# Performance work log

Hardware: AMD Instinct MI355X
Metric: run time of the kernel (lower is better)

The kernel has to match this reference:

```python
import jax, jax.numpy as jnp
import numpy as np

NM = 4096; NP = 4096; EM = 65536; EP = 65536; H = 256; HEADS = 4; G = 32


def _lin(k, din, dout):
    k1, k2 = jax.random.split(k)
    return (jax.random.normal(k1, (din, dout), jnp.float32) * (1.0 / np.sqrt(din)),
            jax.random.normal(k2, (dout,), jnp.float32) * 0.01)


def setup_inputs() -> dict:
    key = jax.random.key(0)
    ks = jax.random.split(key, 32)
    inp = {}
    inp['x_mol'] = jax.random.normal(ks[0], (NM, 8), jnp.float32)
    inp['x_prot'] = jax.random.normal(ks[1], (NP, 4), jnp.float32)
    inp['ea_mol'] = jax.random.normal(ks[2], (EM, 2), jnp.float32)
    inp['ea_prot'] = jax.random.normal(ks[3], (EP, 2), jnp.float32)
    inp['ei_mol'] = jax.random.randint(ks[4], (2, EM), 0, NM)
    inp['ei_prot'] = jax.random.randint(ks[5], (2, EP), 0, NP)
    inp['batch_mol'] = jnp.sort(jax.random.randint(ks[6], (NM,), 0, G))
    inp['batch_prot'] = jnp.sort(jax.random.randint(ks[7], (NP,), 0, G))
    inp['node_lin_mol_w'], inp['node_lin_mol_b'] = _lin(ks[8], 8, H)
    inp['node_lin_prot_w'], inp['node_lin_prot_b'] = _lin(ks[9], 4, H)
    inp['edge_lin_mol_w'], inp['edge_lin_mol_b'] = _lin(ks[10], 2, H)
    inp['edge_lin_prot_w'], inp['edge_lin_prot_b'] = _lin(ks[11], 2, H)
    # two GINE conv layers per graph, each with a 2-layer MLP; stack layer dim first
    for pref, base in (('mol', 12), ('prot', 16)):
        w1 = []; b1 = []; w2 = []; b2 = []
        for l in range(2):
            w, b = _lin(ks[base + 2 * l], H, H); w1.append(w); b1.append(b)
            w, b = _lin(ks[base + 2 * l + 1], H, H); w2.append(w); b2.append(b)
        inp[pref + '_w1'] = jnp.stack(w1); inp[pref + '_b1'] = jnp.stack(b1)
        inp[pref + '_w2'] = jnp.stack(w2); inp[pref + '_b2'] = jnp.stack(b2)
    for pref, base in (('mp', 20), ('pm', 23)):
        inp[pref + '_wq'], inp[pref + '_bq'] = _lin(ks[base], H, H)
        inp[pref + '_wk'], inp[pref + '_bk'] = _lin(ks[base + 1], H, H)
        inp[pref + '_wv'], inp[pref + '_bv'] = _lin(ks[base + 2], H, H)
    inp['fc1_w'], inp['fc1_b'] = _lin(ks[26], 2 * H, H)
    inp['fc2_w'], inp['fc2_b'] = _lin(ks[27], H, 1)
    return inp


def _gine_stack(x, ei, e, w1, b1, w2, b2):
    # GINEConv (eps=0): x_i' = relu(nn(x_i + sum_j relu(x_j + e_ji))), 2 layers, shared edge emb
    src, dst = ei[0], ei[1]
    n = x.shape[0]
    for l in range(w1.shape[0]):
        msg = jax.nn.relu(x[src] + e)                      # [E, H]
        agg = jax.ops.segment_sum(msg, dst, num_segments=n)  # [N, H]
        h = x + agg
        h = jax.nn.relu(h @ w1[l] + b1[l]) @ w2[l] + b2[l]
        x = jax.nn.relu(h)
    return x


def _cross_attn(qn, kn, wq, bq, wk, bk, wv, bv):
    nq, d = qn.shape
    nk = kn.shape[0]
    hd = d // HEADS
    Q = (qn @ wq + bq).reshape(nq, HEADS, hd)
    K = (kn @ wk + bk).reshape(nk, HEADS, hd)
    V = (kn @ wv + bv).reshape(nk, HEADS, hd)
    scores = jnp.einsum('qhd,khd->hqk', Q, K) / np.float32(hd ** 0.5)
    w = jax.nn.softmax(scores, axis=-1)
    return jnp.einsum('hqk,khd->qhd', w, V).reshape(nq, d)


def _seg_mean(h, seg, n):
    s = jax.ops.segment_sum(h, seg, num_segments=n)
    c = jax.ops.segment_sum(jnp.ones((h.shape[0], 1), h.dtype), seg, num_segments=n)
    return s / jnp.maximum(c, 1.0)


def reference(x_mol, x_prot, ea_mol, ea_prot, ei_mol, ei_prot, batch_mol, batch_prot,
              node_lin_mol_w, node_lin_mol_b, node_lin_prot_w, node_lin_prot_b,
              edge_lin_mol_w, edge_lin_mol_b, edge_lin_prot_w, edge_lin_prot_b,
              mol_w1, mol_b1, mol_w2, mol_b2, prot_w1, prot_b1, prot_w2, prot_b2,
              mp_wq, mp_bq, mp_wk, mp_bk, mp_wv, mp_bv,
              pm_wq, pm_bq, pm_wk, pm_bk, pm_wv, pm_bv,
              fc1_w, fc1_b, fc2_w, fc2_b):
    hm = x_mol @ node_lin_mol_w + node_lin_mol_b
    hp = x_prot @ node_lin_prot_w + node_lin_prot_b
    em = ea_mol @ edge_lin_mol_w + edge_lin_mol_b
    ep = ea_prot @ edge_lin_prot_w + edge_lin_prot_b
    H_mol = _gine_stack(hm, ei_mol, em, mol_w1, mol_b1, mol_w2, mol_b2)
    H_prot = _gine_stack(hp, ei_prot, ep, prot_w1, prot_b1, prot_w2, prot_b2)
    H_mol_c = H_mol + _cross_attn(H_mol, H_prot, mp_wq, mp_bq, mp_wk, mp_bk, mp_wv, mp_bv)
    H_prot_c = H_prot + _cross_attn(H_prot, H_mol, pm_wq, pm_bq, pm_wk, pm_bk, pm_wv, pm_bv)
    z_mol = _seg_mean(H_mol_c, batch_mol, G)
    z_prot = _seg_mean(H_prot_c, batch_prot, G)
    z = jnp.concatenate([z_mol, z_prot], axis=1)
    x = jax.nn.relu(z @ fc1_w + fc1_b)
    out = jax.nn.sigmoid(x @ fc2_w + fc2_b)
    return out.squeeze(-1)
```

## Files before the change

kernel.cpp:

```cpp
#include <hip/hip_runtime.h>
#include <math.h>

#define HDIM 256
#define NMOL 4096
#define NPROT 4096
#define NEDGE 65536
#define NG 32

typedef _Float16 f16x8 __attribute__((ext_vector_type(8)));
typedef _Float16 f16x4 __attribute__((ext_vector_type(4)));
typedef __attribute__((ext_vector_type(4))) float f32x4;

__device__ __forceinline__ void splitf(float x, _Float16& h, _Float16& l) {
  h = (_Float16)x;
  l = (_Float16)(x - (float)h);
}

struct PtrPack { const float* p[14]; };

__global__ __launch_bounds__(256) void k_prep_wt(PtrPack pk, _Float16* __restrict__ dh,
                                                 _Float16* __restrict__ dl) {
  __shared__ float Ts[64][68];
  const int m = blockIdx.z;
  const int n0 = blockIdx.y * 64, k0 = blockIdx.x * 64;
  const float* W = pk.p[m];
  const int t = threadIdx.x;
#pragma unroll
  for (int rep = 0; rep < 16; ++rep) {
    int k = rep * 4 + (t >> 6);
    int n = t & 63;
    Ts[n][k] = W[(size_t)(k0 + k) * 256 + n0 + n];
  }
  __syncthreads();
#pragma unroll
  for (int rep = 0; rep < 2; ++rep) {
    int idx = t + rep * 256;
    int nr = idx >> 3, koff = (idx & 7) * 8;
    f16x8 vh, vl;
#pragma unroll
    for (int i = 0; i < 8; ++i) {
      _Float16 h, l;
      splitf(Ts[nr][koff + i], h, l);
      vh[i] = h; vl[i] = l;
    }
    size_t off = (size_t)m * 65536 + (size_t)(n0 + nr) * 256 + k0 + koff;
    *(f16x8*)&dh[off] = vh;
    *(f16x8*)&dl[off] = vl;
  }
}

struct EmbJob { const float* x; const float* w; const float* b; float* out; int K; };

__global__ __launch_bounds__(256) void k_node_embed2(EmbJob j0, EmbJob j1) {
  const EmbJob& j = blockIdx.y ? j1 : j0;
  const int i = blockIdx.x;
  const int c = threadIdx.x;
  float acc = j.b[c];
  for (int k = 0; k < j.K; ++k) acc += j.x[i * j.K + k] * j.w[k * HDIM + c];
  j.out[(size_t)i * HDIM + c] = acc;
}

__global__ __launch_bounds__(256) void k_csr_count2(const int* __restrict__ ei0,
                                                    const int* __restrict__ ei1,
                                                    int* __restrict__ cur0,
                                                    int* __restrict__ cur1, int E) {
  const int* ei = blockIdx.y ? ei1 : ei0;
  int* cur = blockIdx.y ? cur1 : cur0;
  const int e = blockIdx.x * 256 + threadIdx.x;
  if (e < E) atomicAdd(&cur[ei[E + e]], 1);
}

__global__ __launch_bounds__(256) void k_csr_scan2(int* __restrict__ c0, int* __restrict__ o0,
                                                   int* __restrict__ c1, int* __restrict__ o1,
                                                   int N) {
  int* cnt_cur = blockIdx.x ? c1 : c0;
  int* off = blockIdx.x ? o1 : o0;
  __shared__ int tsum[256], tpre[257];
  const int t = threadIdx.x;
  const int base = t * 16;
  int loc[16], s = 0;
#pragma unroll
  for (int i = 0; i < 16; ++i) { loc[i] = cnt_cur[base + i]; s += loc[i]; }
  tsum[t] = s;
  __syncthreads();
  if (t == 0) {
    int a = 0;
    for (int i = 0; i < 256; ++i) { tpre[i] = a; a += tsum[i]; }
    tpre[256] = a;
  }
  __syncthreads();
  int a = tpre[t];
#pragma unroll
  for (int i = 0; i < 16; ++i) {
    off[base + i] = a;
    cnt_cur[base + i] = a;
    a += loc[i];
  }
  if (t == 255) off[N] = tpre[256];
}

__global__ __launch_bounds__(256) void k_csr_scatter2(const int* __restrict__ ei0,
                                                      const int* __restrict__ ei1,
                                                      int* __restrict__ cur0,
                                                      int* __restrict__ cur1,
                                                      int* __restrict__ eid0,
                                                      int* __restrict__ eid1, int E) {
  const int* ei = blockIdx.y ? ei1 : ei0;
  int* cur = blockIdx.y ? cur1 : cur0;
  int* eid = blockIdx.y ? eid1 : eid0;
  const int e = blockIdx.x * 256 + threadIdx.x;
  if (e < E) {
    int pos = atomicAdd(&cur[ei[E + e]], 1);
    eid[pos] = e;
  }
}

struct AggJob {
  const float* x; const float* ea; const int* eis; const int* off;
  const int* eid; const float* we; const float* be; float* agg;
};

__global__ __launch_bounds__(256) void k_agg2(AggJob a0, AggJob a1) {
  const AggJob& a = blockIdx.y ? a1 : a0;
  const int n = blockIdx.x;
  const int c = threadIdx.x;
  const float w0 = a.we[c], w1 = a.we[HDIM + c], bb = a.be[c];
  const int j0 = a.off[n], j1 = a.off[n + 1];
  float sum = 0.f;
  for (int j = j0; j < j1; ++j) {
    int e = a.eid[j];
    int src = a.eis[e];
    float e0 = a.ea[2 * e], e1 = a.ea[2 * e + 1];
    float m = a.x[(size_t)src * HDIM + c] + e0 * w0 + e1 * w1 + bb;
    sum += fmaxf(m, 0.f);
  }
  a.agg[(size_t)n * HDIM + c] = sum;
}

struct GJob {
  const float* A1; const float* A2;
  const _Float16* Ah; const _Float16* Al;
  const _Float16* Bh; const _Float16* Bl;
  const float* bias; float* C;
  _Float16* Ch; _Float16* Cl;
  float oscale; int flags;
};
struct GJobs { GJob j[6]; };

__global__ __launch_bounds__(256) void k_gemm(GJobs js) {
  const GJob J = js.j[blockIdx.z];
  const int relu = J.flags & 1, hasa2 = J.flags & 2, presplit = J.flags & 4;
  const int outmode = J.flags >> 4;
  __shared__ _Float16 Ah[64][72], Al[64][72], Bh[64][72], Bl[64][72];
  const int t = threadIdx.x;
  const int bm = blockIdx.x * 64, bn = blockIdx.y * 64;
  const int lane = t & 63, w = t >> 6;
  const int l15 = lane & 15, l4 = lane >> 4;
  const int wm = (w >> 1) * 32, wn = (w & 1) * 32;
  f32x4 acc[2][2] = {};
  for (int k0 = 0; k0 < 256; k0 += 64) {
    __syncthreads();
    if (presplit) {
#pragma unroll
      for (int rep = 0; rep < 2; ++rep) {
        int idx = t + rep * 256;
        int r = idx >> 3, k8 = (idx & 7) * 8;
        size_t off = (size_t)(bm + r) * 256 + k0 + k8;
        *(f16x8*)&Ah[r][k8] = *(const f16x8*)&J.Ah[off];
        *(f16x8*)&Al[r][k8] = *(const f16x8*)&J.Al[off];
      }
    } else {
#pragma unroll
      for (int rep = 0; rep < 4; ++rep) {
        int idx = t + rep * 256;
        int r = idx >> 4, c4 = (idx & 15) * 4;
        float4 a = *(const float4*)&J.A1[(size_t)(bm + r) * 256 + k0 + c4];
        if (hasa2) {
          float4 a2 = *(const float4*)&J.A2[(size_t)(bm + r) * 256 + k0 + c4];
          a.x += a2.x; a.y += a2.y; a.z += a2.z; a.w += a2.w;
        }
        float av[4] = {a.x, a.y, a.z, a.w};
#pragma unroll
        for (int i = 0; i < 4; ++i) splitf(av[i], Ah[r][c4 + i], Al[r][c4 + i]);
      }
    }
#pragma unroll
    for (int rep = 0; rep < 2; ++rep) {
      int idx = t + rep * 256;
      int nr = idx >> 3, koff = (idx & 7) * 8;
      size_t off = (size_t)(bn + nr) * 256 + k0 + koff;
      *(f16x8*)&Bh[nr][koff] = *(const f16x8*)&J.Bh[off];
      *(f16x8*)&Bl[nr][koff] = *(const f16x8*)&J.Bl[off];
    }
    __syncthreads();
#pragma unroll
    for (int kh = 0; kh < 2; ++kh) {
      f16x8 a0h = *(f16x8*)&Ah[wm + l15][kh * 32 + l4 * 8];
      f16x8 a0l = *(f16x8*)&Al[wm + l15][kh * 32 + l4 * 8];
      f16x8 a1h = *(f16x8*)&Ah[wm + 16 + l15][kh * 32 + l4 * 8];
      f16x8 a1l = *(f16x8*)&Al[wm + 16 + l15][kh * 32 + l4 * 8];
      f16x8 b0h = *(f16x8*)&Bh[wn + l15][kh * 32 + l4 * 8];
      f16x8 b0l = *(f16x8*)&Bl[wn + l15][kh * 32 + l4 * 8];
      f16x8 b1h = *(f16x8*)&Bh[wn + 16 + l15][kh * 32 + l4 * 8];
      f16x8 b1l = *(f16x8*)&Bl[wn + 16 + l15][kh * 32 + l4 * 8];
      acc[0][0] = __builtin_amdgcn_mfma_f32_16x16x32_f16(a0h, b0h, acc[0][0], 0, 0, 0);
      acc[0][0] = __builtin_amdgcn_mfma_f32_16x16x32_f16(a0h, b0l, acc[0][0], 0, 0, 0);
      acc[0][0] = __builtin_amdgcn_mfma_f32_16x16x32_f16(a0l, b0h, acc[0][0], 0, 0, 0);
      acc[0][1] = __builtin_amdgcn_mfma_f32_16x16x32_f16(a0h, b1h, acc[0][1], 0, 0, 0);
      acc[0][1] = __builtin_amdgcn_mfma_f32_16x16x32_f16(a0h, b1l, acc[0][1], 0, 0, 0);
      acc[0][1] = __builtin_amdgcn_mfma_f32_16x16x32_f16(a0l, b1h, acc[0][1], 0, 0, 0);
      acc[1][0] = __builtin_amdgcn_mfma_f32_16x16x32_f16(a1h, b0h, acc[1][0], 0, 0, 0);
      acc[1][0] = __builtin_amdgcn_mfma_f32_16x16x32_f16(a1h, b0l, acc[1][0], 0, 0, 0);
      acc[1][0] = __builtin_amdgcn_mfma_f32_16x16x32_f16(a1l, b0h, acc[1][0], 0, 0, 0);
      acc[1][1] = __builtin_amdgcn_mfma_f32_16x16x32_f16(a1h, b1h, acc[1][1], 0, 0, 0);
      acc[1][1] = __builtin_amdgcn_mfma_f32_16x16x32_f16(a1h, b1l, acc[1][1], 0, 0, 0);
      acc[1][1] = __builtin_amdgcn_mfma_f32_16x16x32_f16(a1l, b1h, acc[1][1], 0, 0, 0);
    }
  }
#pragma unroll
  for (int mi = 0; mi < 2; ++mi)
#pragma unroll
    for (int ni = 0; ni < 2; ++ni) {
      int col = bn + wn + ni * 16 + l15;
      float bv = J.bias[col];
#pragma unroll
      for (int r = 0; r < 4; ++r) {
        int row = bm + wm + mi * 16 + l4 * 4 + r;
        float v = acc[mi][ni][r] + bv;
        if (relu) v = fmaxf(v, 0.f);
        if (outmode != 1) J.C[(size_t)row * 256 + col] = v;
        if (outmode != 0) {
          float vs = v * J.oscale;
          _Float16 hh, ll;
          splitf(vs, hh, ll);
          J.Ch[(size_t)row * 256 + col] = hh;
          J.Cl[(size_t)row * 256 + col] = ll;
        }
      }
    }
}

__global__ __launch_bounds__(256) void k_transpose2(
    const float* __restrict__ V0, const float* __restrict__ V1,
    _Float16* __restrict__ Th0, _Float16* __restrict__ Th1) {
  __shared__ float Ts[64][65];
  const int dir = blockIdx.z;
  const float* V = dir ? V1 : V0;
  _Float16* Th = dir ? Th1 : Th0;
  const int r0 = blockIdx.x * 64, c0 = blockIdx.y * 64;
  const int t = threadIdx.x;
#pragma unroll
  for (int rep = 0; rep < 16; ++rep) {
    int idx = rep * 256 + t;
    int r = idx >> 6, c = idx & 63;
    Ts[r][c] = V[(size_t)(r0 + r) * 256 + c0 + c];
  }
  __syncthreads();
#pragma unroll
  for (int rep = 0; rep < 2; ++rep) {
    int idx = rep * 256 + t;
    int c = idx >> 3, r8 = (idx & 7) * 8;
    f16x8 vh;
#pragma unroll
    for (int i = 0; i < 8; ++i) vh[i] = (_Float16)Ts[r8 + i][c];
    *(f16x8*)&Th[(size_t)(c0 + c) * 4096 + r0 + r8] = vh;
  }
}

struct AttnArgs {
  const _Float16* Qh[2]; const _Float16* Ql[2];
  const _Float16* Kh[2]; const _Float16* Kl[2];
  const _Float16* Vth[2];
  float* Opart; float* mpart; float* lpart;
};

__global__ __launch_bounds__(256) void k_attn4(AttnArgs A, int nk_half) {
  __shared__ _Float16 Ksh[64][72], Ksl[64][72];
  __shared__ _Float16 Vsh[64][72];
  __shared__ _Float16 Psh[4][16][72];
  const int t = threadIdx.x;
  const int dir = blockIdx.y >> 2, h = blockIdx.y & 3;
  const int q0 = blockIdx.x * 64;
  const int half = blockIdx.z;
  const int kbase = half * nk_half;
  const int lane = t & 63, w = t >> 6;
  const int l15 = lane & 15, l4 = lane >> 4;

  const _Float16* Qh_g = A.Qh[dir];
  const _Float16* Ql_g = A.Ql[dir];
  const _Float16* Kh_g = A.Kh[dir];
  const _Float16* Kl_g = A.Kl[dir];
  const _Float16* Vth_g = A.Vth[dir];

  f16x8 qh[2], ql[2];
  {
    size_t qoff = (size_t)(q0 + w * 16 + l15) * 256 + h * 64;
#pragma unroll
    for (int kh = 0; kh < 2; ++kh) {
      qh[kh] = *(const f16x8*)&Qh_g[qoff + kh * 32 + l4 * 8];
      ql[kh] = *(const f16x8*)&Ql_g[qoff + kh * 32 + l4 * 8];
    }
  }
  f32x4 o[4] = {};
  float mrun = -1e30f;
  float lrun = 0.f;

  for (int kt = 0; kt < nk_half; kt += 64) {
    const int k0 = kbase + kt;
    __syncthreads();
#pragma unroll
    for (int rep = 0; rep < 2; ++rep) {
      int idx = t + rep * 256;
      int r = idx >> 3, c8 = idx & 7;
      size_t koff = (size_t)(k0 + r) * 256 + h * 64 + c8 * 8;
      *(f16x8*)&Ksh[r][c8 * 8] = *(const f16x8*)&Kh_g[koff];
      *(f16x8*)&Ksl[r][c8 * 8] = *(const f16x8*)&Kl_g[koff];
      int sc = c8 ^ ((r >> 3) & 7);
      size_t voff = (size_t)(h * 64 + r) * 4096 + k0 + c8 * 8;
      *(f16x8*)&Vsh[r][sc * 8] = *(const f16x8*)&Vth_g[voff];
    }
    __syncthreads();

    f32x4 sf[4] = {};
#pragma unroll
    for (int kc = 0; kc < 4; ++kc) {
      f16x8 kf0h = *(f16x8*)&Ksh[kc * 16 + l15][l4 * 8];
      f16x8 kf0l = *(f16x8*)&Ksl[kc * 16 + l15][l4 * 8];
      f16x8 kf1h = *(f16x8*)&Ksh[kc * 16 + l15][32 + l4 * 8];
      f16x8 kf1l = *(f16x8*)&Ksl[kc * 16 + l15][32 + l4 * 8];
      sf[kc] = __builtin_amdgcn_mfma_f32_16x16x32_f16(kf0h, qh[0], sf[kc], 0, 0, 0);
      sf[kc] = __builtin_amdgcn_mfma_f32_16x16x32_f16(kf0h, ql[0], sf[kc], 0, 0, 0);
      sf[kc] = __builtin_amdgcn_mfma_f32_16x16x32_f16(kf0l, qh[0], sf[kc], 0, 0, 0);
      sf[kc] = __builtin_amdgcn_mfma_f32_16x16x32_f16(kf1h, qh[1], sf[kc], 0, 0, 0);
      sf[kc] = __builtin_amdgcn_mfma_f32_16x16x32_f16(kf1h, ql[1], sf[kc], 0, 0, 0);
      sf[kc] = __builtin_amdgcn_mfma_f32_16x16x32_f16(kf1l, qh[1], sf[kc], 0, 0, 0);
    }

    float mt = -1e30f;
#pragma unroll
    for (int kc = 0; kc < 4; ++kc) {
      float a = fmaxf(fmaxf(sf[kc][0], sf[kc][1]), fmaxf(sf[kc][2], sf[kc][3]));
      mt = fmaxf(mt, a);
    }
    mt = fmaxf(mt, __shfl_xor(mt, 16, 64));
    mt = fmaxf(mt, __shfl_xor(mt, 32, 64));
    float mn = fmaxf(mrun, mt);
    float alpha = __expf(mrun - mn);
    mrun = mn;
    float rs = 0.f;
    _Float16 pf[4][4];
#pragma unroll
    for (int kc = 0; kc < 4; ++kc)
#pragma unroll
      for (int r = 0; r < 4; ++r) {
        float pv = __expf(sf[kc][r] - mn);
        rs += pv;
        pf[kc][r] = (_Float16)pv;
      }
    rs += __shfl_xor(rs, 16, 64);
    rs += __shfl_xor(rs, 32, 64);
    lrun = lrun * alpha + rs;

#pragma unroll
    for (int r = 0; r < 4; ++r) {
      float ar = __shfl(alpha, 4 * l4 + r, 64);
      o[0][r] *= ar; o[1][r] *= ar; o[2][r] *= ar; o[3][r] *= ar;
    }

#pragma unroll
    for (int kc = 0; kc < 4; ++kc) {
      f16x4 pv = {pf[kc][0], pf[kc][1], pf[kc][2], pf[kc][3]};
      *(f16x4*)&Psh[w][l15][kc * 16 + 4 * l4] = pv;
    }

#pragma unroll
    for (int kh = 0; kh < 2; ++kh) {
      f16x8 pa = *(f16x8*)&Psh[w][l15][kh * 32 + l4 * 8];
#pragma unroll
      for (int oc = 0; oc < 4; ++oc) {
        int d = oc * 16 + l15;
        int chunk = (kh * 4 + l4) ^ ((d >> 3) & 7);
        f16x8 vb = *(f16x8*)&Vsh[d][chunk * 8];
        o[oc] = __builtin_amdgcn_mfma_f32_16x16x32_f16(pa, vb, o[oc], 0, 0, 0);
      }
    }
  }

  const int slot = dir * 2 + half;
#pragma unroll
  for (int oc = 0; oc < 4; ++oc) {
    int col = h * 64 + oc * 16 + l15;
#pragma unroll
    for (int r = 0; r < 4; ++r) {
      int row = q0 + w * 16 + 4 * l4 + r;
      A.Opart[((size_t)slot * 4096 + row) * 256 + col] = o[oc][r];
    }
  }
  if (lane < 16) {
    int row = q0 + w * 16 + l15;
    A.mpart[(size_t)(slot * 4 + h) * 4096 + row] = mrun;
    A.lpart[(size_t)(slot * 4 + h) * 4096 + row] = lrun;
  }
}

__global__ __launch_bounds__(256) void k_combine_pool(
    const float* __restrict__ Opart, const float* __restrict__ mpart,
    const float* __restrict__ lpart, const float* __restrict__ hm,
    const float* __restrict__ hp, const int* __restrict__ b_mol,
    const int* __restrict__ b_prot, float* __restrict__ z, float* __restrict__ cnt) {
  const int row = blockIdx.x;
  const int dir = blockIdx.y;
  const int c = threadIdx.x;
  const int h = c >> 6;
  const float* Hin = dir ? hp : hm;
  const int g = (dir ? b_prot : b_mol)[row];
  size_t mi0 = (size_t)((dir * 2 + 0) * 4 + h) * 4096 + row;
  size_t mi1 = (size_t)((dir * 2 + 1) * 4 + h) * 4096 + row;
  float m1 = mpart[mi0], m2 = mpart[mi1];
  float l1 = lpart[mi0], l2 = lpart[mi1];
  float M = fmaxf(m1, m2);
  float e1 = __expf(m1 - M), e2 = __expf(m2 - M);
  float L = l1 * e1 + l2 * e2;
  float O1 = Opart[((size_t)(dir * 2 + 0) * 4096 + row) * 256 + c];
  float O2 = Opart[((size_t)(dir * 2 + 1) * 4096 + row) * 256 + c];
  float v = (O1 * e1 + O2 * e2) / L + Hin[(size_t)row * 256 + c];
  atomicAdd(&z[(size_t)g * 512 + dir * 256 + c], v);
  if (c == 0) atomicAdd(&cnt[dir * 32 + g], 1.0f);
}

__global__ __launch_bounds__(256) void k_segdiv(float* __restrict__ z,
                                                const float* __restrict__ cnt) {
  const int idx = blockIdx.x * 256 + threadIdx.x;
  const int g = idx >> 9, c = idx & 511;
  const float cc = cnt[(c < 256) ? g : (32 + g)];
  z[idx] /= fmaxf(cc, 1.0f);
}

__global__ __launch_bounds__(256) void k_fc1(
    const float* __restrict__ z, const float* __restrict__ w,
    const float* __restrict__ b, float* __restrict__ out) {
  const int idx = blockIdx.x * 256 + threadIdx.x;
  const int r = idx >> 8, c = idx & 255;
  float acc = b[c];
  for (int k = 0; k < 512; ++k) acc += z[r * 512 + k] * w[k * HDIM + c];
  out[idx] = fmaxf(acc, 0.f);
}

__global__ __launch_bounds__(64) void k_fc2(
    const float* __restrict__ xin, const float* __restrict__ w,
    const float* __restrict__ b, float* __restrict__ out) {
  const int r = threadIdx.x;
  if (r < NG) {
    float acc = b[0];
    for (int k = 0; k < HDIM; ++k) acc += xin[r * HDIM + k] * w[k];
    out[r] = 1.0f / (1.0f + __expf(-acc));
  }
}

extern "C" void kernel_launch(void* const* d_in, const int* in_sizes, int n_in,
                              void* d_out, int out_size, void* d_ws, size_t ws_size,
                              hipStream_t stream) {
  const float* x_mol   = (const float*)d_in[0];
  const float* x_prot  = (const float*)d_in[1];
  const float* ea_mol  = (const float*)d_in[2];
  const float* ea_prot = (const float*)d_in[3];
  const int*   ei_mol  = (const int*)d_in[4];
  const int*   ei_prot = (const int*)d_in[5];
  const int*   b_mol   = (const int*)d_in[6];
  const int*   b_prot  = (const int*)d_in[7];
  const float* nlm_w = (const float*)d_in[8];
  const float* nlm_b = (const float*)d_in[9];
  const float* nlp_w = (const float*)d_in[10];
  const float* nlp_b = (const float*)d_in[11];
  const float* elm_w = (const float*)d_in[12];
  const float* elm_b = (const float*)d_in[13];
  const float* elp_w = (const float*)d_in[14];
  const float* elp_b = (const float*)d_in[15];
  const float* mol_w1 = (const float*)d_in[16];
  const float* mol_b1 = (const float*)d_in[17];
  const float* mol_w2 = (const float*)d_in[18];
  const float* mol_b2 = (const float*)d_in[19];
  const float* prot_w1 = (const float*)d_in[20];
  const float* prot_b1 = (const float*)d_in[21];
  const float* prot_w2 = (const float*)d_in[22];
  const float* prot_b2 = (const float*)d_in[23];
  const float* mp_wq = (const float*)d_in[24];
  const float* mp_bq = (const float*)d_in[25];
  const float* mp_wk = (const float*)d_in[26];
  const float* mp_bk = (const float*)d_in[27];
  const float* mp_wv = (const float*)d_in[28];
  const float* mp_bv = (const float*)d_in[29];
  const float* pm_wq = (const float*)d_in[30];
  const float* pm_bq = (const float*)d_in[31];
  const float* pm_wk = (const float*)d_in[32];
  const float* pm_bk = (const float*)d_in[33];
  const float* pm_wv = (const float*)d_in[34];
  const float* pm_bv = (const float*)d_in[35];
  const float* fc1_w = (const float*)d_in[36];
  const float* fc1_b = (const float*)d_in[37];
  const float* fc2_w = (const float*)d_in[38];
  const float* fc2_b = (const float*)d_in[39];
  float* out = (float*)d_out;

  char* W8 = (char*)d_ws;
  const size_t MB = 1u << 20;
  float* hm    = (float*)(W8 + 0 * MB);
  float* hp    = (float*)(W8 + 4 * MB);
  float* t1m   = (float*)(W8 + 8 * MB);
  float* aggm  = (float*)(W8 + 12 * MB);
  float* aggp  = (float*)(W8 + 16 * MB);
  _Float16* wtH = (_Float16*)(W8 + 20 * MB);
  _Float16* wtL = (_Float16*)(W8 + 22 * MB);
  _Float16* hmh = (_Float16*)(W8 + 24 * MB);
  _Float16* hml = (_Float16*)(W8 + 26 * MB);
  _Float16* hph = (_Float16*)(W8 + 28 * MB);
  _Float16* hpl = (_Float16*)(W8 + 30 * MB);
  _Float16* Qh0 = (_Float16*)(W8 + 32 * MB);
  _Float16* Ql0 = (_Float16*)(W8 + 34 * MB);
  _Float16* Kh0 = (_Float16*)(W8 + 36 * MB);
  _Float16* Kl0 = (_Float16*)(W8 + 38 * MB);
  _Float16* Qh1 = (_Float16*)(W8 + 40 * MB);
  _Float16* Ql1 = (_Float16*)(W8 + 42 * MB);
  _Float16* Kh1 = (_Float16*)(W8 + 44 * MB);
  _Float16* Kl1 = (_Float16*)(W8 + 46 * MB);
  float* Vb0   = (float*)(W8 + 48 * MB);
  float* Vb1   = (float*)(W8 + 52 * MB);
  _Float16* Vth0 = (_Float16*)(W8 + 56 * MB);
  _Float16* Vth1 = (_Float16*)(W8 + 60 * MB);
  float* Opart = (float*)(W8 + 64 * MB);
  float* mpart = (float*)(W8 + 80 * MB);
  float* lpart = mpart + 65536;
  float* zb    = lpart + 65536;
  float* cnt   = zb + 32 * 512;
  float* fch   = cnt + 64;
  float* t1p   = (float*)(W8 + 82 * MB);
  int* off_m = (int*)(W8 + 86 * MB);
  int* cur_m = off_m + 4224;
  int* eid_m = cur_m + 4224;
  int* off_p = (int*)(W8 + 87 * MB);
  int* cur_p = off_p + 4224;
  int* eid_p = cur_p + 4224;

  PtrPack pk;
  pk.p[0] = mol_w1;           pk.p[1] = mol_w1 + 65536;
  pk.p[2] = mol_w2;           pk.p[3] = mol_w2 + 65536;
  pk.p[4] = prot_w1;          pk.p[5] = prot_w1 + 65536;
  pk.p[6] = prot_w2;          pk.p[7] = prot_w2 + 65536;
  pk.p[8] = mp_wq;  pk.p[9] = mp_wk;  pk.p[10] = mp_wv;
  pk.p[11] = pm_wq; pk.p[12] = pm_wk; pk.p[13] = pm_wv;
  k_prep_wt<<<dim3(4, 4, 14), 256, 0, stream>>>(pk, wtH, wtL);

  hipMemsetAsync(cur_m, 0, 4096 * 4, stream);
  hipMemsetAsync(cur_p, 0, 4096 * 4, stream);
  k_csr_count2<<<dim3(NEDGE / 256, 2), 256, 0, stream>>>(ei_mol, ei_prot, cur_m, cur_p, NEDGE);
  k_csr_scan2<<<2, 256, 0, stream>>>(cur_m, off_m, cur_p, off_p, NMOL);
  k_csr_scatter2<<<dim3(NEDGE / 256, 2), 256, 0, stream>>>(ei_mol, ei_prot, cur_m, cur_p,
                                                           eid_m, eid_p, NEDGE);

  EmbJob em = {x_mol, nlm_w, nlm_b, hm, 8};
  EmbJob ep = {x_prot, nlp_w, nlp_b, hp, 4};
  k_node_embed2<<<dim3(NMOL, 2), 256, 0, stream>>>(em, ep);

#define WTH(i) (wtH + (size_t)(i) * 65536)
#define WTL(i) (wtL + (size_t)(i) * 65536)

  AggJob am = {hm, ea_mol, ei_mol, off_m, eid_m, elm_w, elm_b, aggm};
  AggJob ap = {hp, ea_prot, ei_prot, off_p, eid_p, elp_w, elp_b, aggp};

  for (int l = 0; l < 2; ++l) {
    k_agg2<<<dim3(NMOL, 2), 256, 0, stream>>>(am, ap);
    GJobs g1 = {};
    g1.j[0] = {hm, aggm, nullptr, nullptr, WTH(l), WTL(l), mol_b1 + l * 256,
               t1m, nullptr, nullptr, 1.0f, 3};
    g1.j[1] = {hp, aggp, nullptr, nullptr, WTH(4 + l), WTL(4 + l), prot_b1 + l * 256,
               t1p, nullptr, nullptr, 1.0f, 3};
    k_gemm<<<dim3(64, 4, 2), 256, 0, stream>>>(g1);
    GJobs g2 = {};
    int fl = (l == 1) ? (1 | (2 << 4)) : 1;
    g2.j[0] = {t1m, nullptr, nullptr, nullptr, WTH(2 + l), WTL(2 + l), mol_b2 + l * 256,
               hm, hmh, hml, 1.0f, fl};
    g2.j[1] = {t1p, nullptr, nullptr, nullptr, WTH(6 + l), WTL(6 + l), prot_b2 + l * 256,
               hp, hph, hpl, 1.0f, fl};
    k_gemm<<<dim3(64, 4, 2), 256, 0, stream>>>(g2);
  }

  {
    GJobs q = {};
    q.j[0] = {nullptr, nullptr, hmh, hml, WTH(8), WTL(8), mp_bq,
              nullptr, Qh0, Ql0, 0.125f, 4 | (1 << 4)};
    q.j[1] = {nullptr, nullptr, hph, hpl, WTH(9), WTL(9), mp_bk,
              nullptr, Kh0, Kl0, 1.0f, 4 | (1 << 4)};
    q.j[2] = {nullptr, nullptr, hph, hpl, WTH(10), WTL(10), mp_bv,
              Vb0, nullptr, nullptr, 1.0f, 4};
    q.j[3] = {nullptr, nullptr, hph, hpl, WTH(11), WTL(11), pm_bq,
              nullptr, Qh1, Ql1, 0.125f, 4 | (1 << 4)};
    q.j[4] = {nullptr, nullptr, hmh, hml, WTH(12), WTL(12), pm_bk,
              nullptr, Kh1, Kl1, 1.0f, 4 | (1 << 4)};
    q.j[5] = {nullptr, nullptr, hmh, hml, WTH(13), WTL(13), pm_bv,
              Vb1, nullptr, nullptr, 1.0f, 4};
    k_gemm<<<dim3(64, 4, 6), 256, 0, stream>>>(q);
  }

  k_transpose2<<<dim3(64, 4, 2), 256, 0, stream>>>(Vb0, Vb1, Vth0, Vth1);

  AttnArgs aa;
  aa.Qh[0] = Qh0; aa.Ql[0] = Ql0; aa.Kh[0] = Kh0; aa.Kl[0] = Kl0; aa.Vth[0] = Vth0;
  aa.Qh[1] = Qh1; aa.Ql[1] = Ql1; aa.Kh[1] = Kh1; aa.Kl[1] = Kl1; aa.Vth[1] = Vth1;
  aa.Opart = Opart; aa.mpart = mpart; aa.lpart = lpart;
  k_attn4<<<dim3(64, 8, 2), 256, 0, stream>>>(aa, 2048);

  hipMemsetAsync(zb, 0, (32 * 512 + 64) * 4, stream);
  k_combine_pool<<<dim3(4096, 2), 256, 0, stream>>>(Opart, mpart, lpart, hm, hp,
                                                    b_mol, b_prot, zb, cnt);
  k_segdiv<<<64, 256, 0, stream>>>(zb, cnt);
  k_fc1<<<32, 256, 0, stream>>>(zb, fc1_w, fc1_b, fch);
  k_fc2<<<1, 64, 0, stream>>>(fch, fc2_w, fc2_b, out);
#undef WTH
#undef WTL
}
```

Before: 546.0 us.

## Keep activations in split fp16 hi/lo form and fuse V transpose into GEMM

Node features, aggregation results and MLP intermediates are now stored as fp16 hi/lo pairs instead of fp32. The GEMM therefore always loads presplit operands and drops the fp32 split path. The self-term addition moves into the aggregation kernel. The V projection writes its transposed fp16 output directly through shared memory, which removes the separate transpose kernel and the fp32 V buffers. This cuts global traffic and one launch, at the cost of extra conversion arithmetic in the gather loop and a small precision change from hi/lo reconstruction.

```diff
diff --git a/kernel.cpp b/kernel.cpp
--- a/kernel.cpp
+++ b/kernel.cpp
@@ -49,7 +49,10 @@
   }
 }
 
-struct EmbJob { const float* x; const float* w; const float* b; float* out; int K; };
+struct EmbJob {
+  const float* x; const float* w; const float* b;
+  _Float16* oh; _Float16* ol; int K;
+};
 
 __global__ __launch_bounds__(256) void k_node_embed2(EmbJob j0, EmbJob j1) {
   const EmbJob& j = blockIdx.y ? j1 : j0;
@@ -57,7 +60,10 @@
   const int c = threadIdx.x;
   float acc = j.b[c];
   for (int k = 0; k < j.K; ++k) acc += j.x[i * j.K + k] * j.w[k * HDIM + c];
-  j.out[(size_t)i * HDIM + c] = acc;
+  _Float16 h, l;
+  splitf(acc, h, l);
+  j.oh[(size_t)i * HDIM + c] = h;
+  j.ol[(size_t)i * HDIM + c] = l;
 }
 
 __global__ __launch_bounds__(256) void k_csr_count2(const int* __restrict__ ei0,
@@ -116,8 +122,10 @@
 }
 
 struct AggJob {
-  const float* x; const float* ea; const int* eis; const int* off;
-  const int* eid; const float* we; const float* be; float* agg;
+  const _Float16* xh; const _Float16* xl; const float* ea;
+  const int* eis; const int* off; const int* eid;
+  const float* we; const float* be;
+  _Float16* sh; _Float16* sl;
 };
 
 __global__ __launch_bounds__(256) void k_agg2(AggJob a0, AggJob a1) {
@@ -131,25 +139,29 @@
     int e = a.eid[j];
     int src = a.eis[e];
     float e0 = a.ea[2 * e], e1 = a.ea[2 * e + 1];
-    float m = a.x[(size_t)src * HDIM + c] + e0 * w0 + e1 * w1 + bb;
+    float xv = (float)a.xh[(size_t)src * HDIM + c] + (float)a.xl[(size_t)src * HDIM + c];
+    float m = xv + e0 * w0 + e1 * w1 + bb;
     sum += fmaxf(m, 0.f);
   }
-  a.agg[(size_t)n * HDIM + c] = sum;
+  float self = (float)a.xh[(size_t)n * HDIM + c] + (float)a.xl[(size_t)n * HDIM + c];
+  _Float16 h, l;
+  splitf(self + sum, h, l);
+  a.sh[(size_t)n * HDIM + c] = h;
+  a.sl[(size_t)n * HDIM + c] = l;
 }
 
 struct GJob {
-  const float* A1; const float* A2;
   const _Float16* Ah; const _Float16* Al;
   const _Float16* Bh; const _Float16* Bl;
-  const float* bias; float* C;
-  _Float16* Ch; _Float16* Cl;
+  const float* bias;
+  _Float16* Ch; _Float16* Cl; _Float16* Vt;
   float oscale; int flags;
 };
 struct GJobs { GJob j[6]; };
 
 __global__ __launch_bounds__(256) void k_gemm(GJobs js) {
   const GJob J = js.j[blockIdx.z];
-  const int relu = J.flags & 1, hasa2 = J.flags & 2, presplit = J.flags & 4;
+  const int relu = J.flags & 1;
   const int outmode = J.flags >> 4;
   __shared__ _Float16 Ah[64][72], Al[64][72], Bh[64][72], Bl[64][72];
   const int t = threadIdx.x;
@@ -160,37 +172,16 @@
   f32x4 acc[2][2] = {};
   for (int k0 = 0; k0 < 256; k0 += 64) {
     __syncthreads();
-    if (presplit) {
-#pragma unroll
-      for (int rep = 0; rep < 2; ++rep) {
-        int idx = t + rep * 256;
-        int r = idx >> 3, k8 = (idx & 7) * 8;
-        size_t off = (size_t)(bm + r) * 256 + k0 + k8;
-        *(f16x8*)&Ah[r][k8] = *(const f16x8*)&J.Ah[off];
-        *(f16x8*)&Al[r][k8] = *(const f16x8*)&J.Al[off];
-      }
-    } else {
-#pragma unroll
-      for (int rep = 0; rep < 4; ++rep) {
-        int idx = t + rep * 256;
-        int r = idx >> 4, c4 = (idx & 15) * 4;
-        float4 a = *(const float4*)&J.A1[(size_t)(bm + r) * 256 + k0 + c4];
-        if (hasa2) {
-          float4 a2 = *(const float4*)&J.A2[(size_t)(bm + r) * 256 + k0 + c4];
-          a.x += a2.x; a.y += a2.y; a.z += a2.z; a.w += a2.w;
-        }
-        float av[4] = {a.x, a.y, a.z, a.w};
-#pragma unroll
-        for (int i = 0; i < 4; ++i) splitf(av[i], Ah[r][c4 + i], Al[r][c4 + i]);
-      }
-    }
 #pragma unroll
     for (int rep = 0; rep < 2; ++rep) {
       int idx = t + rep * 256;
-      int nr = idx >> 3, koff = (idx & 7) * 8;
-      size_t off = (size_t)(bn + nr) * 256 + k0 + koff;
-      *(f16x8*)&Bh[nr][koff] = *(const f16x8*)&J.Bh[off];
-      *(f16x8*)&Bl[nr][koff] = *(const f16x8*)&J.Bl[off];
+      int r = idx >> 3, k8 = (idx & 7) * 8;
+      size_t offa = (size_t)(bm + r) * 256 + k0 + k8;
+      *(f16x8*)&Ah[r][k8] = *(const f16x8*)&J.Ah[offa];
+      *(f16x8*)&Al[r][k8] = *(const f16x8*)&J.Al[offa];
+      size_t offb = (size_t)(bn + r) * 256 + k0 + k8;
+      *(f16x8*)&Bh[r][k8] = *(const f16x8*)&J.Bh[offb];
+      *(f16x8*)&Bl[r][k8] = *(const f16x8*)&J.Bl[offb];
     }
     __syncthreads();
 #pragma unroll
@@ -217,6 +208,7 @@
       acc[1][1] = __builtin_amdgcn_mfma_f32_16x16x32_f16(a1l, b1h, acc[1][1], 0, 0, 0);
     }
   }
+  if (outmode == 3) __syncthreads();
 #pragma unroll
   for (int mi = 0; mi < 2; ++mi)
 #pragma unroll
@@ -228,42 +220,25 @@
         int row = bm + wm + mi * 16 + l4 * 4 + r;
         float v = acc[mi][ni][r] + bv;
         if (relu) v = fmaxf(v, 0.f);
-        if (outmode != 1) J.C[(size_t)row * 256 + col] = v;
-        if (outmode != 0) {
+        if (outmode == 1) {
           float vs = v * J.oscale;
           _Float16 hh, ll;
           splitf(vs, hh, ll);
           J.Ch[(size_t)row * 256 + col] = hh;
           J.Cl[(size_t)row * 256 + col] = ll;
+        } else {
+          Ah[wn + ni * 16 + l15][wm + mi * 16 + l4 * 4 + r] = (_Float16)v;
         }
       }
     }
-}
-
-__global__ __launch_bounds__(256) void k_transpose2(
-    const float* __restrict__ V0, const float* __restrict__ V1,
-    _Float16* __restrict__ Th0, _Float16* __restrict__ Th1) {
-  __shared__ float Ts[64][65];
-  const int dir = blockIdx.z;
-  const float* V = dir ? V1 : V0;
-  _Float16* Th = dir ? Th1 : Th0;
-  const int r0 = blockIdx.x * 64, c0 = blockIdx.y * 64;
-  const int t = threadIdx.x;
-#pragma unroll
-  for (int rep = 0; rep < 16; ++rep) {
-    int idx = rep * 256 + t;
-    int r = idx >> 6, c = idx & 63;
-    Ts[r][c] = V[(size_t)(r0 + r) * 256 + c0 + c];
-  }
-  __syncthreads();
-#pragma unroll
-  for (int rep = 0; rep < 2; ++rep) {
-    int idx = rep * 256 + t;
-    int c = idx >> 3, r8 = (idx & 7) * 8;
-    f16x8 vh;
-#pragma unroll
-    for (int i = 0; i < 8; ++i) vh[i] = (_Float16)Ts[r8 + i][c];
-    *(f16x8*)&Th[(size_t)(c0 + c) * 4096 + r0 + r8] = vh;
+  if (outmode == 3) {
+    __syncthreads();
+#pragma unroll
+    for (int rep = 0; rep < 2; ++rep) {
+      int idx = t + rep * 256;
+      int d = idx >> 3, n8 = (idx & 7) * 8;
+      *(f16x8*)&J.Vt[(size_t)(bn + d) * 4096 + bm + n8] = *(f16x8*)&Ah[d][n8];
+    }
   }
 }
 
@@ -405,14 +380,17 @@
 
 __global__ __launch_bounds__(256) void k_combine_pool(
     const float* __restrict__ Opart, const float* __restrict__ mpart,
-    const float* __restrict__ lpart, const float* __restrict__ hm,
-    const float* __restrict__ hp, const int* __restrict__ b_mol,
-    const int* __restrict__ b_prot, float* __restrict__ z, float* __restrict__ cnt) {
+    const float* __restrict__ lpart,
+    const _Float16* __restrict__ hmh, const _Float16* __restrict__ hml,
+    const _Float16* __restrict__ hph, const _Float16* __restrict__ hpl,
+    const int* __restrict__ b_mol, const int* __restrict__ b_prot,
+    float* __restrict__ z, float* __restrict__ cnt) {
   const int row = blockIdx.x;
   const int dir = blockIdx.y;
   const int c = threadIdx.x;
   const int h = c >> 6;
-  const float* Hin = dir ? hp : hm;
+  const _Float16* Hh = dir ? hph : hmh;
+  const _Float16* Hl = dir ? hpl : hml;
   const int g = (dir ? b_prot : b_mol)[row];
   size_t mi0 = (size_t)((dir * 2 + 0) * 4 + h) * 4096 + row;
   size_t mi1 = (size_t)((dir * 2 + 1) * 4 + h) * 4096 + row;
@@ -423,7 +401,8 @@
   float L = l1 * e1 + l2 * e2;
   float O1 = Opart[((size_t)(dir * 2 + 0) * 4096 + row) * 256 + c];
   float O2 = Opart[((size_t)(dir * 2 + 1) * 4096 + row) * 256 + c];
-  float v = (O1 * e1 + O2 * e2) / L + Hin[(size_t)row * 256 + c];
+  float hin = (float)Hh[(size_t)row * 256 + c] + (float)Hl[(size_t)row * 256 + c];
+  float v = (O1 * e1 + O2 * e2) / L + hin;
   atomicAdd(&z[(size_t)g * 512 + dir * 256 + c], v);
   if (c == 0) atomicAdd(&cnt[dir * 32 + g], 1.0f);
 }
@@ -504,40 +483,40 @@
 
   char* W8 = (char*)d_ws;
   const size_t MB = 1u << 20;
-  float* hm    = (float*)(W8 + 0 * MB);
-  float* hp    = (float*)(W8 + 4 * MB);
-  float* t1m   = (float*)(W8 + 8 * MB);
-  float* aggm  = (float*)(W8 + 12 * MB);
-  float* aggp  = (float*)(W8 + 16 * MB);
-  _Float16* wtH = (_Float16*)(W8 + 20 * MB);
-  _Float16* wtL = (_Float16*)(W8 + 22 * MB);
-  _Float16* hmh = (_Float16*)(W8 + 24 * MB);
-  _Float16* hml = (_Float16*)(W8 + 26 * MB);
-  _Float16* hph = (_Float16*)(W8 + 28 * MB);
-  _Float16* hpl = (_Float16*)(W8 + 30 * MB);
-  _Float16* Qh0 = (_Float16*)(W8 + 32 * MB);
-  _Float16* Ql0 = (_Float16*)(W8 + 34 * MB);
-  _Float16* Kh0 = (_Float16*)(W8 + 36 * MB);
-  _Float16* Kl0 = (_Float16*)(W8 + 38 * MB);
-  _Float16* Qh1 = (_Float16*)(W8 + 40 * MB);
-  _Float16* Ql1 = (_Float16*)(W8 + 42 * MB);
-  _Float16* Kh1 = (_Float16*)(W8 + 44 * MB);
-  _Float16* Kl1 = (_Float16*)(W8 + 46 * MB);
-  float* Vb0   = (float*)(W8 + 48 * MB);
-  float* Vb1   = (float*)(W8 + 52 * MB);
-  _Float16* Vth0 = (_Float16*)(W8 + 56 * MB);
-  _Float16* Vth1 = (_Float16*)(W8 + 60 * MB);
-  float* Opart = (float*)(W8 + 64 * MB);
-  float* mpart = (float*)(W8 + 80 * MB);
+  _Float16* wtH  = (_Float16*)(W8 + 0 * MB);
+  _Float16* wtL  = (_Float16*)(W8 + 2 * MB);
+  _Float16* hmh  = (_Float16*)(W8 + 4 * MB);
+  _Float16* hml  = (_Float16*)(W8 + 6 * MB);
+  _Float16* hph  = (_Float16*)(W8 + 8 * MB);
+  _Float16* hpl  = (_Float16*)(W8 + 10 * MB);
+  _Float16* amh  = (_Float16*)(W8 + 12 * MB);
+  _Float16* aml  = (_Float16*)(W8 + 14 * MB);
+  _Float16* aph  = (_Float16*)(W8 + 16 * MB);
+  _Float16* apl  = (_Float16*)(W8 + 18 * MB);
+  _Float16* t1mh = (_Float16*)(W8 + 20 * MB);
+  _Float16* t1ml = (_Float16*)(W8 + 22 * MB);
+  _Float16* t1ph = (_Float16*)(W8 + 24 * MB);
+  _Float16* t1pl = (_Float16*)(W8 + 26 * MB);
+  _Float16* Qh0  = (_Float16*)(W8 + 28 * MB);
+  _Float16* Ql0  = (_Float16*)(W8 + 30 * MB);
+  _Float16* Kh0  = (_Float16*)(W8 + 32 * MB);
+  _Float16* Kl0  = (_Float16*)(W8 + 34 * MB);
+  _Float16* Qh1  = (_Float16*)(W8 + 36 * MB);
+  _Float16* Ql1  = (_Float16*)(W8 + 38 * MB);
+  _Float16* Kh1  = (_Float16*)(W8 + 40 * MB);
+  _Float16* Kl1  = (_Float16*)(W8 + 42 * MB);
+  _Float16* Vth0 = (_Float16*)(W8 + 44 * MB);
+  _Float16* Vth1 = (_Float16*)(W8 + 46 * MB);
+  float* Opart = (float*)(W8 + 48 * MB);
+  float* mpart = (float*)(W8 + 64 * MB);
   float* lpart = mpart + 65536;
   float* zb    = lpart + 65536;
   float* cnt   = zb + 32 * 512;
   float* fch   = cnt + 64;
-  float* t1p   = (float*)(W8 + 82 * MB);
-  int* off_m = (int*)(W8 + 86 * MB);
+  int* off_m = (int*)(W8 + 65 * MB);
   int* cur_m = off_m + 4224;
   int* eid_m = cur_m + 4224;
-  int* off_p = (int*)(W8 + 87 * MB);
+  int* off_p = (int*)(W8 + 66 * MB);
   int* cur_p = off_p + 4224;
   int* eid_p = cur_p + 4224;
 
@@ -557,51 +536,42 @@
   k_csr_scatter2<<<dim3(NEDGE / 256, 2), 256, 0, stream>>>(ei_mol, ei_prot, cur_m, cur_p,
                                                            eid_m, eid_p, NEDGE);
 
-  EmbJob em = {x_mol, nlm_w, nlm_b, hm, 8};
-  EmbJob ep = {x_prot, nlp_w, nlp_b, hp, 4};
+  EmbJob em = {x_mol, nlm_w, nlm_b, hmh, hml, 8};
+  EmbJob ep = {x_prot, nlp_w, nlp_b, hph, hpl, 4};
   k_node_embed2<<<dim3(NMOL, 2), 256, 0, stream>>>(em, ep);
 
 #define WTH(i) (wtH + (size_t)(i) * 65536)
 #define WTL(i) (wtL + (size_t)(i) * 65536)
 
-  AggJob am = {hm, ea_mol, ei_mol, off_m, eid_m, elm_w, elm_b, aggm};
-  AggJob ap = {hp, ea_prot, ei_prot, off_p, eid_p, elp_w, elp_b, aggp};
+  AggJob am = {hmh, hml, ea_mol, ei_mol, off_m, eid_m, elm_w, elm_b, amh, aml};
+  AggJob ap = {hph, hpl, ea_prot, ei_prot, off_p, eid_p, elp_w, elp_b, aph, apl};
 
   for (int l = 0; l < 2; ++l) {
     k_agg2<<<dim3(NMOL, 2), 256, 0, stream>>>(am, ap);
     GJobs g1 = {};
-    g1.j[0] = {hm, aggm, nullptr, nullptr, WTH(l), WTL(l), mol_b1 + l * 256,
-               t1m, nullptr, nullptr, 1.0f, 3};
-    g1.j[1] = {hp, aggp, nullptr, nullptr, WTH(4 + l), WTL(4 + l), prot_b1 + l * 256,
-               t1p, nullptr, nullptr, 1.0f, 3};
+    g1.j[0] = {amh, aml, WTH(l), WTL(l), mol_b1 + l * 256,
+               t1mh, t1ml, nullptr, 1.0f, 1 | (1 << 4)};
+    g1.j[1] = {aph, apl, WTH(4 + l), WTL(4 + l), prot_b1 + l * 256,
+               t1ph, t1pl, nullptr, 1.0f, 1 | (1 << 4)};
     k_gemm<<<dim3(64, 4, 2), 256, 0, stream>>>(g1);
     GJobs g2 = {};
-    int fl = (l == 1) ? (1 | (2 << 4)) : 1;
-    g2.j[0] = {t1m, nullptr, nullptr, nullptr, WTH(2 + l), WTL(2 + l), mol_b2 + l * 256,
-               hm, hmh, hml, 1.0f, fl};
-    g2.j[1] = {t1p, nullptr, nullptr, nullptr, WTH(6 + l), WTL(6 + l), prot_b2 + l * 256,
-               hp, hph, hpl, 1.0f, fl};
+    g2.j[0] = {t1mh, t1ml, WTH(2 + l), WTL(2 + l), mol_b2 + l * 256,
+               hmh, hml, nullptr, 1.0f, 1 | (1 << 4)};
+    g2.j[1] = {t1ph, t1pl, WTH(6 + l), WTL(6 + l), prot_b2 + l * 256,
+               hph, hpl, nullptr, 1.0f, 1 | (1 << 4)};
     k_gemm<<<dim3(64, 4, 2), 256, 0, stream>>>(g2);
   }
 
   {
     GJobs q = {};
-    q.j[0] = {nullptr, nullptr, hmh, hml, WTH(8), WTL(8), mp_bq,
-              nullptr, Qh0, Ql0, 0.125f, 4 | (1 << 4)};
-    q.j[1] = {nullptr, nullptr, hph, hpl, WTH(9), WTL(9), mp_bk,
-              nullptr, Kh0, Kl0, 1.0f, 4 | (1 << 4)};
-    q.j[2] = {nullptr, nullptr, hph, hpl, WTH(10), WTL(10), mp_bv,
-              Vb0, nullptr, nullptr, 1.0f, 4};
-    q.j[3] = {nullptr, nullptr, hph, hpl, WTH(11), WTL(11), pm_bq,
-              nullptr, Qh1, Ql1, 0.125f, 4 | (1 << 4)};
-    q.j[4] = {nullptr, nullptr, hmh, hml, WTH(12), WTL(12), pm_bk,
-              nullptr, Kh1, Kl1, 1.0f, 4 | (1 << 4)};
-    q.j[5] = {nullptr, nullptr, hmh, hml, WTH(13), WTL(13), pm_bv,
-              Vb1, nullptr, nullptr, 1.0f, 4};
+    q.j[0] = {hmh, hml, WTH(8), WTL(8), mp_bq, Qh0, Ql0, nullptr, 0.125f, 1 << 4};
+    q.j[1] = {hph, hpl, WTH(9), WTL(9), mp_bk, Kh0, Kl0, nullptr, 1.0f, 1 << 4};
+    q.j[2] = {hph, hpl, WTH(10), WTL(10), mp_bv, nullptr, nullptr, Vth0, 1.0f, 3 << 4};
+    q.j[3] = {hph, hpl, WTH(11), WTL(11), pm_bq, Qh1, Ql1, nullptr, 0.125f, 1 << 4};
+    q.j[4] = {hmh, hml, WTH(12), WTL(12), pm_bk, Kh1, Kl1, nullptr, 1.0f, 1 << 4};
+    q.j[5] = {hmh, hml, WTH(13), WTL(13), pm_bv, nullptr, nullptr, Vth1, 1.0f, 3 << 4};
     k_gemm<<<dim3(64, 4, 6), 256, 0, stream>>>(q);
   }
-
-  k_transpose2<<<dim3(64, 4, 2), 256, 0, stream>>>(Vb0, Vb1, Vth0, Vth1);
 
   AttnArgs aa;
   aa.Qh[0] = Qh0; aa.Ql[0] = Ql0; aa.Kh[0] = Kh0; aa.Kl[0] = Kl0; aa.Vth[0] = Vth0;
@@ -610,7 +580,8 @@
   k_attn4<<<dim3(64, 8, 2), 256, 0, stream>>>(aa, 2048);
 
   hipMemsetAsync(zb, 0, (32 * 512 + 64) * 4, stream);
-  k_combine_pool<<<dim3(4096, 2), 256, 0, stream>>>(Opart, mpart, lpart, hm, hp,
+  k_combine_pool<<<dim3(4096, 2), 256, 0, stream>>>(Opart, mpart, lpart,
+                                                    hmh, hml, hph, hpl,
                                                     b_mol, b_prot, zb, cnt);
   k_segdiv<<<64, 256, 0, stream>>>(zb, cnt);
   k_fc1<<<32, 256, 0, stream>>>(zb, fc1_w, fc1_b, fch);
```

Measured after the change: 535.2 us. -2.0%, faster.
